# Performance work log

Hardware: AMD Instinct MI355X
Metric: run time of the kernel (lower is better)

## Reference

```python
import jax, jax.numpy as jnp
import numpy as np

IMG_W = 256; IMG_H = 256; N_PTS = 320
MIN_DEPTH = 3.0; MAX_DEPTH = 9.0; NDC_EXTENT = 1.0
SCALING = 0.1; EA_EPS = 1e-10; NORM_EPS = 1e-8


def setup_inputs() -> dict:
    key = jax.random.key(0)
    B, D = 1, 256
    image3d = jax.random.uniform(key, (B, 1, D, D, D), dtype=jnp.float32)
    # PyTorch3D convention: X_cam = X_world @ R + T. Camera at z=-6 world looking at origin.
    R = jnp.tile(jnp.eye(3, dtype=jnp.float32)[None], (B, 1, 1))
    T = jnp.tile(jnp.array([[0.0, 0.0, 6.0]], dtype=jnp.float32), (B, 1))
    focal = jnp.full((B,), 1.7320508, dtype=jnp.float32)  # NDC focal, fov ~ 60deg
    return {"image3d": image3d, "R": R, "T": T, "focal": focal}


def _trilinear_sample(vol, pts):
    # vol: [C, D, H, W]; pts: [N, 3] in xyz order, normalized coords in [-1, 1]
    # (grid_sample semantics: align_corners=True, padding_mode='zeros')
    C, D, H, W = vol.shape
    sizes = jnp.array([W, H, D], dtype=pts.dtype)
    idx = (pts + 1.0) * 0.5 * (sizes - 1.0)
    i0f = jnp.floor(idx)
    frac = idx - i0f
    i0 = i0f.astype(jnp.int32)
    volf = vol.reshape(C, -1)
    out = jnp.zeros((C, pts.shape[0]), dtype=vol.dtype)
    for dz in (0, 1):
        for dy in (0, 1):
            for dx in (0, 1):
                ix = i0[:, 0] + dx; iy = i0[:, 1] + dy; iz = i0[:, 2] + dz
                w = ((frac[:, 0] if dx else 1.0 - frac[:, 0]) *
                     (frac[:, 1] if dy else 1.0 - frac[:, 1]) *
                     (frac[:, 2] if dz else 1.0 - frac[:, 2]))
                valid = (ix >= 0) & (ix < W) & (iy >= 0) & (iy < H) & (iz >= 0) & (iz < D)
                lin = (jnp.clip(iz, 0, D - 1) * H + jnp.clip(iy, 0, H - 1)) * W + jnp.clip(ix, 0, W - 1)
                out = out + jnp.where(valid, w, 0.0)[None, :] * volf[:, lin]
    return out


def reference(image3d, R, T, focal):
    B, Cin, D, H, W = image3d.shape
    # features = image3d.repeat(1,3,1,1,1) when single channel
    features = jnp.broadcast_to(image3d, (B, 3, D, H, W)) if Cin == 1 else image3d
    densities = jnp.ones_like(image3d[:, :1]) * SCALING  # [B,1,D,H,W]
    shape = max(Cin, D)
    voxel_size = 2.0 * NDC_EXTENT / shape
    # Volumes local coords: world extent voxel_size*(size-1) maps to [-1,1]
    half_extent = jnp.array([voxel_size * (W - 1) / 2.0,
                             voxel_size * (H - 1) / 2.0,
                             voxel_size * (D - 1) / 2.0], dtype=image3d.dtype)
    # NDC pixel-center grid (PyTorch3D: +x left, +y up)
    xs = jnp.linspace(1.0 - 1.0 / IMG_W, -(1.0 - 1.0 / IMG_W), IMG_W, dtype=image3d.dtype)
    ys = jnp.linspace(1.0 - 1.0 / IMG_H, -(1.0 - 1.0 / IMG_H), IMG_H, dtype=image3d.dtype)
    depths = jnp.linspace(MIN_DEPTH, MAX_DEPTH, N_PTS, dtype=image3d.dtype)
    gy, gx = jnp.meshgrid(ys, xs, indexing="ij")  # [Hi, Wi]
    f = focal[:, None, None, None]
    dd = depths[None, None, None, :]
    x_cam = gx[None, :, :, None] * dd / f
    y_cam = gy[None, :, :, None] * dd / f
    z_cam = jnp.broadcast_to(dd, x_cam.shape)
    pts_cam = jnp.stack([x_cam, y_cam, z_cam], axis=-1)  # [B, Hi, Wi, P, 3]
    # unproject: X_world = (X_cam - T) @ R^T, i.e. X_world_i = sum_j (Xc - T)_j R_ij
    pts_world = jnp.einsum('bhwpj,bij->bhwpi', pts_cam - T[:, None, None, None, :], R)
    pts_local = pts_world / half_extent
    vol = jnp.concatenate([features, densities], axis=1)  # [B, 4, D, H, W]
    N = IMG_H * IMG_W * N_PTS
    vals = jax.vmap(_trilinear_sample)(vol, pts_local.reshape(B, N, 3))  # [B, 4, N]
    vals = vals.reshape(B, 4, IMG_H, IMG_W, N_PTS)
    feats = vals[:, :3]           # [B, 3, Hi, Wi, P]
    dens = vals[:, 3]             # [B, Hi, Wi, P]
    # EmissionAbsorption raymarcher: shifted cumprod absorption, alpha compositing
    cp = jnp.cumprod((1.0 + EA_EPS) - dens, axis=-1)
    absorption = jnp.concatenate([jnp.ones_like(cp[..., :1]), cp[..., :-1]], axis=-1)
    weights = dens * absorption
    rgb = jnp.einsum('bhwp,bchwp->bhwc', weights, feats)      # [B, Hi, Wi, 3]
    opacity = 1.0 - jnp.prod(1.0 - dens, axis=-1)             # [B, Hi, Wi]
    rgba = jnp.concatenate([rgb, opacity[..., None]], axis=-1)  # [B, Hi, Wi, 4]
    screen = jnp.transpose(rgba, (0, 3, 2, 1))                # [B, 4, Wi, Hi]
    gray = screen.mean(axis=1, keepdims=True)                 # is_grayscale=True
    return (gray + NORM_EPS) / (gray.max() + NORM_EPS)        # minimized()
```

## Files before the change

kernel.cpp:

```cpp
#include <hip/hip_runtime.h>

#define IMG_W 256
#define IMG_H 256
#define N_PTS 320
#define VD 256
#define VH 256
#define VW 256
#define NCHUNK 4
#define PPC (N_PTS / NCHUNK)

__global__ __launch_bounds__(256) void render_kernel(
    const float* __restrict__ vol,
    const float* __restrict__ Rm,
    const float* __restrict__ Tv,
    const float* __restrict__ focal,
    float* __restrict__ out,
    unsigned int* __restrict__ maxbits)
{
    const int tx = threadIdx.x;
    const int ty = threadIdx.y;
    const int w  = blockIdx.x * 64 + tx;
    const int h  = blockIdx.y;

    const float a  = 1.0f - 1.0f / IMG_W;
    const float gx = a - (2.0f * a / (IMG_W - 1)) * (float)w;
    const float gy = a - (2.0f * a / (IMG_H - 1)) * (float)h;

    const float f  = focal[0];
    const float ux = gx / f, uy = gy / f;

    const float R00 = Rm[0], R01 = Rm[1], R02 = Rm[2];
    const float R10 = Rm[3], R11 = Rm[4], R12 = Rm[5];
    const float R20 = Rm[6], R21 = Rm[7], R22 = Rm[8];
    const float Tx = Tv[0], Ty = Tv[1], Tz = Tv[2];

    const float Bx = R00 * ux + R01 * uy + R02;
    const float By = R10 * ux + R11 * uy + R12;
    const float Bz = R20 * ux + R21 * uy + R22;
    const float Ax = -(R00 * Tx + R01 * Ty + R02 * Tz);
    const float Ay = -(R10 * Tx + R11 * Ty + R12 * Tz);
    const float Az = -(R20 * Tx + R21 * Ty + R22 * Tz);

    const float voxel = 2.0f / 256.0f;
    const float hx = voxel * (VW - 1) * 0.5f;
    const float hy = voxel * (VH - 1) * 0.5f;
    const float hz = voxel * (VD - 1) * 0.5f;

    const float sxc = 0.5f * (VW - 1) / hx, oxc = 0.5f * (VW - 1);
    const float syc = 0.5f * (VH - 1) / hy, oyc = 0.5f * (VH - 1);
    const float szc = 0.5f * (VD - 1) / hz, ozc = 0.5f * (VD - 1);
    const float fBx = Bx * sxc, fAx = Ax * sxc + oxc;
    const float fBy = By * syc, fAy = Ay * syc + oyc;
    const float fBz = Bz * szc, fAz = Az * szc + ozc;

    const float dstep = 6.0f / (N_PTS - 1);

    float S = 0.0f;
    float A = 1.0f;

    #pragma unroll 4
    for (int i = 0; i < PPC; ++i) {
        const int   p = ty * PPC + i;
        const float d = 3.0f + (float)p * dstep;

        const float fx = fmaf(fBx, d, fAx);
        const float fy = fmaf(fBy, d, fAy);
        const float fz = fmaf(fBz, d, fAz);

        const float flx = floorf(fx), fly = floorf(fy), flz = floorf(fz);
        const int ix0 = (int)flx, iy0 = (int)fly, iz0 = (int)flz;

        float dens = 0.0f, feat = 0.0f;
        if (ix0 >= -1 && ix0 < VW && iy0 >= -1 && iy0 < VH && iz0 >= -1 && iz0 < VD) {
            const float frx = fx - flx, fry = fy - fly, frz = fz - flz;
            float wx0 = 1.0f - frx, wx1 = frx;
            float wy0 = 1.0f - fry, wy1 = fry;
            float wz0 = 1.0f - frz, wz1 = frz;
            if (ix0 < 0)       wx0 = 0.0f;
            if (ix0 + 1 >= VW) wx1 = 0.0f;
            if (iy0 < 0)       wy0 = 0.0f;
            if (iy0 + 1 >= VH) wy1 = 0.0f;
            if (iz0 < 0)       wz0 = 0.0f;
            if (iz0 + 1 >= VD) wz1 = 0.0f;

            const int cx0 = max(ix0, 0), cx1 = min(ix0 + 1, VW - 1);
            const int cy0 = max(iy0, 0), cy1 = min(iy0 + 1, VH - 1);
            const int cz0 = max(iz0, 0), cz1 = min(iz0 + 1, VD - 1);

            const int zb0 = cz0 * (VH * VW), zb1 = cz1 * (VH * VW);
            const int yb0 = cy0 * VW,        yb1 = cy1 * VW;

            const float v000 = vol[zb0 + yb0 + cx0];
            const float v001 = vol[zb0 + yb0 + cx1];
            const float v010 = vol[zb0 + yb1 + cx0];
            const float v011 = vol[zb0 + yb1 + cx1];
            const float v100 = vol[zb1 + yb0 + cx0];
            const float v101 = vol[zb1 + yb0 + cx1];
            const float v110 = vol[zb1 + yb1 + cx0];
            const float v111 = vol[zb1 + yb1 + cx1];

            const float w00 = wy0 * wz0, w01 = wy1 * wz0;
            const float w10 = wy0 * wz1, w11 = wy1 * wz1;
            const float c000 = wx0 * w00, c001 = wx1 * w00;
            const float c010 = wx0 * w01, c011 = wx1 * w01;
            const float c100 = wx0 * w10, c101 = wx1 * w10;
            const float c110 = wx0 * w11, c111 = wx1 * w11;

            feat = c000 * v000 + c001 * v001 + c010 * v010 + c011 * v011
                 + c100 * v100 + c101 * v101 + c110 * v110 + c111 * v111;
            dens = 0.1f * (c000 + c001 + c010 + c011 + c100 + c101 + c110 + c111);
        }

        S = fmaf(dens * A, feat, S);
        A *= (1.0f - dens);
    }

    __shared__ float lS[NCHUNK][64];
    __shared__ float lA[NCHUNK][64];
    lS[ty][tx] = S;
    lA[ty][tx] = A;
    __syncthreads();

    if (ty == 0) {
        const float S0 = lS[0][tx], S1 = lS[1][tx], S2 = lS[2][tx], S3 = lS[3][tx];
        const float A0 = lA[0][tx], A1 = lA[1][tx], A2 = lA[2][tx], A3 = lA[3][tx];
        const float Stot = S0 + A0 * (S1 + A1 * (S2 + A2 * S3));
        const float Atot = A0 * A1 * A2 * A3;
        const float gray = (3.0f * Stot + (1.0f - Atot)) * 0.25f;
        out[w * IMG_H + h] = gray;

        float m = gray;
        #pragma unroll
        for (int off = 32; off > 0; off >>= 1)
            m = fmaxf(m, __shfl_down(m, off));
        if (tx == 0)
            atomicMax(maxbits, __float_as_uint(m));
    }
}

__global__ __launch_bounds__(256) void normalize_kernel(
    float* __restrict__ out, const unsigned int* __restrict__ maxbits)
{
    const int i = blockIdx.x * blockDim.x + threadIdx.x;
    const float m = __uint_as_float(*maxbits);
    out[i] = (out[i] + 1e-8f) / (m + 1e-8f);
}

extern "C" void kernel_launch(void* const* d_in, const int* in_sizes, int n_in,
                              void* d_out, int out_size, void* d_ws, size_t ws_size,
                              hipStream_t stream) {
    (void)in_sizes; (void)n_in; (void)out_size; (void)ws_size;
    const float* vol   = (const float*)d_in[0];
    const float* Rm    = (const float*)d_in[1];
    const float* Tv    = (const float*)d_in[2];
    const float* focal = (const float*)d_in[3];
    float* out = (float*)d_out;
    unsigned int* maxbits = (unsigned int*)d_ws;

    hipMemsetAsync(d_ws, 0, 4, stream);

    dim3 block(64, NCHUNK, 1);
    dim3 grid(IMG_W / 64, IMG_H, 1);
    render_kernel<<<grid, block, 0, stream>>>(vol, Rm, Tv, focal, out, maxbits);

    normalize_kernel<<<(IMG_W * IMG_H) / 256, 256, 0, stream>>>(out, maxbits);
}
```

Before: 129.5 us.

## Clip ray samples to volume bounding box and split range across 32 chunks

Each pixel intersects its ray with the volume's slab bounds and only marches sample indices inside the box, skipping samples that would contribute zero. The surviving range is split across 32 threads per pixel, with 8 pixels per block, and the partial results are composited in shared memory. This removes wasted samples outside the volume, at the cost of less coalesced gather patterns, uneven work between chunks, and a longer serial combine step.

```diff
diff --git a/kernel.cpp b/kernel.cpp
--- a/kernel.cpp
+++ b/kernel.cpp
@@ -6,8 +6,9 @@
 #define VD 256
 #define VH 256
 #define VW 256
-#define NCHUNK 4
-#define PPC (N_PTS / NCHUNK)
+#define PX 8
+#define NC 32
+#define DSTEP (6.0f / (N_PTS - 1))
 
 __global__ __launch_bounds__(256) void render_kernel(
     const float* __restrict__ vol,
@@ -19,7 +20,7 @@
 {
     const int tx = threadIdx.x;
     const int ty = threadIdx.y;
-    const int w  = blockIdx.x * 64 + tx;
+    const int w  = blockIdx.x * PX + tx;
     const int h  = blockIdx.y;
 
     const float a  = 1.0f - 1.0f / IMG_W;
@@ -53,15 +54,40 @@
     const float fBy = By * syc, fAy = Ay * syc + oyc;
     const float fBz = Bz * szc, fAz = Az * szc + ozc;
 
-    const float dstep = 6.0f / (N_PTS - 1);
+    float dlo = 3.0f, dhi = 9.0f;
+    {
+        const float lo = -1.0f, hi = 256.0f;
+        #pragma unroll
+        for (int dim = 0; dim < 3; ++dim) {
+            const float fA = dim == 0 ? fAx : (dim == 1 ? fAy : fAz);
+            const float fB = dim == 0 ? fBx : (dim == 1 ? fBy : fBz);
+            if (fabsf(fB) > 1e-12f) {
+                const float r = 1.0f / fB;
+                const float t0 = (lo - fA) * r, t1 = (hi - fA) * r;
+                dlo = fmaxf(dlo, fminf(t0, t1));
+                dhi = fminf(dhi, fmaxf(t0, t1));
+            } else if (fA < lo || fA >= hi) {
+                dhi = -1.0f;
+            }
+        }
+    }
+    int pmin = 0, pmax = 0;
+    if (dhi > dlo) {
+        pmin = max(0, (int)floorf((dlo - 3.0f) / DSTEP) - 1);
+        pmax = min(N_PTS, (int)ceilf((dhi - 3.0f) / DSTEP) + 2);
+        if (pmax < pmin) pmax = pmin;
+    }
+
+    const int len = pmax - pmin;
+    const int plo = pmin + ((len * ty) >> 5);
+    const int phi = pmin + ((len * (ty + 1)) >> 5);
 
     float S = 0.0f;
     float A = 1.0f;
 
-    #pragma unroll 4
-    for (int i = 0; i < PPC; ++i) {
-        const int   p = ty * PPC + i;
-        const float d = 3.0f + (float)p * dstep;
+    #pragma unroll 2
+    for (int p = plo; p < phi; ++p) {
+        const float d = 3.0f + (float)p * DSTEP;
 
         const float fx = fmaf(fBx, d, fAx);
         const float fy = fmaf(fBy, d, fAy);
@@ -115,25 +141,27 @@
         A *= (1.0f - dens);
     }
 
-    __shared__ float lS[NCHUNK][64];
-    __shared__ float lA[NCHUNK][64];
+    __shared__ float lS[NC][PX];
+    __shared__ float lA[NC][PX];
     lS[ty][tx] = S;
     lA[ty][tx] = A;
     __syncthreads();
 
     if (ty == 0) {
-        const float S0 = lS[0][tx], S1 = lS[1][tx], S2 = lS[2][tx], S3 = lS[3][tx];
-        const float A0 = lA[0][tx], A1 = lA[1][tx], A2 = lA[2][tx], A3 = lA[3][tx];
-        const float Stot = S0 + A0 * (S1 + A1 * (S2 + A2 * S3));
-        const float Atot = A0 * A1 * A2 * A3;
+        float Stot = 0.0f, Atot = 1.0f;
+        #pragma unroll
+        for (int c = 0; c < NC; ++c) {
+            Stot = fmaf(Atot, lS[c][tx], Stot);
+            Atot *= lA[c][tx];
+        }
         const float gray = (3.0f * Stot + (1.0f - Atot)) * 0.25f;
         out[w * IMG_H + h] = gray;
 
         float m = gray;
-        #pragma unroll
-        for (int off = 32; off > 0; off >>= 1)
-            m = fmaxf(m, __shfl_down(m, off));
-        if (tx == 0)
+        m = fmaxf(m, __shfl_down(m, 4));
+        m = fmaxf(m, __shfl_down(m, 2));
+        m = fmaxf(m, __shfl_down(m, 1));
+        if (tx == 0 && m > 0.0f)
             atomicMax(maxbits, __float_as_uint(m));
     }
 }
@@ -159,8 +187,8 @@
 
     hipMemsetAsync(d_ws, 0, 4, stream);
 
-    dim3 block(64, NCHUNK, 1);
-    dim3 grid(IMG_W / 64, IMG_H, 1);
+    dim3 block(PX, NC, 1);
+    dim3 grid(IMG_W / PX, IMG_H, 1);
     render_kernel<<<grid, block, 0, stream>>>(vol, Rm, Tv, focal, out, maxbits);
 
     normalize_kernel<<<(IMG_W * IMG_H) / 256, 256, 0, stream>>>(out, maxbits);
```

Measured after the change: 115.1 us. 1.12x faster.
